# Kernel optimization log

Hardware: AMD Instinct MI355X
Metric: run time of the kernel (lower is better)

## Reference

```python
import jax, jax.numpy as jnp
import numpy as np

B, T, F = 1024, 512, 32
H, E, L = 128, 16, 2
N_TICKERS = 5000


def _gru_layer(x_seq, W_ih, W_hh, b_ih, b_hh):
    # x_seq: [B, T, I]; W_ih: [3H, I]; W_hh: [3H, H]. PyTorch gate order: r, z, n.
    gx = jnp.einsum('bti,gi->btg', x_seq, W_ih) + b_ih  # [B, T, 3H]

    def step(h, gx_t):
        gh = h @ W_hh.T + b_hh                     # [B, 3H]
        r = jax.nn.sigmoid(gx_t[:, :H] + gh[:, :H])
        z = jax.nn.sigmoid(gx_t[:, H:2 * H] + gh[:, H:2 * H])
        n = jnp.tanh(gx_t[:, 2 * H:] + r * gh[:, 2 * H:])
        h_new = (1.0 - z) * n + z * h
        return h_new, h_new

    h0 = jnp.zeros((x_seq.shape[0], H), dtype=x_seq.dtype)
    _, hs = jax.lax.scan(step, h0, jnp.swapaxes(gx, 0, 1))  # hs: [T, B, H]
    return jnp.swapaxes(hs, 0, 1)                            # [B, T, H]


def setup_inputs() -> dict:
    key = jax.random.key(0)
    ks = jax.random.split(key, 16)
    s_in0 = 1.0 / np.sqrt(H)
    inp = {
        'x': jax.random.normal(ks[0], (B, T, F), dtype=jnp.float32),
        'ticker_ids': jax.random.randint(ks[1], (B,), 0, N_TICKERS),
        'embed': jax.random.normal(ks[2], (N_TICKERS, E), dtype=jnp.float32),
        # GRU layer 0 (input size F+E=48)
        'W_ih0': jax.random.uniform(ks[3], (3 * H, F + E), minval=-s_in0, maxval=s_in0),
        'W_hh0': jax.random.uniform(ks[4], (3 * H, H), minval=-s_in0, maxval=s_in0),
        'b_ih0': jax.random.uniform(ks[5], (3 * H,), minval=-s_in0, maxval=s_in0),
        'b_hh0': jax.random.uniform(ks[6], (3 * H,), minval=-s_in0, maxval=s_in0),
        # GRU layer 1 (input size H)
        'W_ih1': jax.random.uniform(ks[7], (3 * H, H), minval=-s_in0, maxval=s_in0),
        'W_hh1': jax.random.uniform(ks[8], (3 * H, H), minval=-s_in0, maxval=s_in0),
        'b_ih1': jax.random.uniform(ks[9], (3 * H,), minval=-s_in0, maxval=s_in0),
        'b_hh1': jax.random.uniform(ks[10], (3 * H,), minval=-s_in0, maxval=s_in0),
        # head: Linear(H,H) -> ReLU -> Linear(H,1)
        'head_w1': jax.random.uniform(ks[11], (H, H), minval=-s_in0, maxval=s_in0),
        'head_b1': jax.random.uniform(ks[12], (H,), minval=-s_in0, maxval=s_in0),
        'head_w2': jax.random.uniform(ks[13], (1, H), minval=-s_in0, maxval=s_in0),
        'head_b2': jax.random.uniform(ks[14], (1,), minval=-s_in0, maxval=s_in0),
    }
    return inp


def reference(x, ticker_ids, embed, W_ih0, W_hh0, b_ih0, b_hh0,
              W_ih1, W_hh1, b_ih1, b_hh1, head_w1, head_b1, head_w2, head_b2):
    emb = embed[ticker_ids]                                  # [B, E]
    emb_seq = jnp.broadcast_to(emb[:, None, :], (x.shape[0], x.shape[1], emb.shape[-1]))
    xcat = jnp.concatenate([x, emb_seq], axis=-1)            # [B, T, F+E]
    h = _gru_layer(xcat, W_ih0, W_hh0, b_ih0, b_hh0)         # [B, T, H]
    h = _gru_layer(h, W_ih1, W_hh1, b_ih1, b_hh1)            # [B, T, H]
    last = h[:, -1, :]                                       # [B, H]
    hid = jax.nn.relu(last @ head_w1.T + head_b1)            # dropout inactive at eval
    y = (hid @ head_w2.T + head_b2)[:, 0]                    # [B]
    return y
```

## Files before the change

kernel.cpp:

```cpp
#include <hip/hip_runtime.h>

constexpr int kB  = 1024;
constexpr int kT  = 512;
constexpr int kF  = 32;
constexpr int kE  = 16;
constexpr int kH  = 128;
constexpr int kMB = 16;
constexpr int kNMB = kB / kMB;
constexpr int kTc = 16;
constexpr int kNCh = kT / kTc;
constexpr int kTg = kTc / 2;
constexpr size_t kH0Str = (size_t)kB * kTc * kH;
constexpr size_t kSlots = (size_t)kNMB * kTc * 512;
constexpr size_t kGx0Str = kSlots * 12;

typedef __attribute__((ext_vector_type(8))) _Float16 f16x8;
typedef __attribute__((ext_vector_type(4))) _Float16 f16x4;
typedef __attribute__((ext_vector_type(4))) float    f32x4;

#define MFMA16(a,b,c) __builtin_amdgcn_mfma_f32_16x16x32_f16(a,b,c,0,0,0)

__device__ __forceinline__ float sigm_hw(float x){
    float e = __builtin_amdgcn_exp2f(-1.442695041f * x);
    return __builtin_amdgcn_rcpf(1.0f + e);
}
__device__ __forceinline__ float tanh_hw(float x){
    float e = __builtin_amdgcn_exp2f(-2.885390082f * x);
    return fmaf(2.0f, __builtin_amdgcn_rcpf(1.0f + e), -1.0f);
}
__device__ __forceinline__ void splitF(float v, _Float16 &hi, _Float16 &lo){
    hi = (_Float16)v;
    lo = (_Float16)(v - (float)hi);
}
__device__ __forceinline__ f16x8 loadW8(const float* __restrict__ p){
    f16x8 r;
#pragma unroll
    for (int j=0;j<8;j++) r[j] = (_Float16)p[j];
    return r;
}
__device__ __forceinline__ unsigned short f2u(_Float16 h){ return __builtin_bit_cast(unsigned short, h); }
__device__ __forceinline__ _Float16 u2f(unsigned short u){ return __builtin_bit_cast(_Float16, u); }
__device__ __forceinline__ unsigned pack2(float a, float b){
    return (unsigned)f2u((_Float16)a) | ((unsigned)f2u((_Float16)b) << 16);
}
__device__ __forceinline__ float uf(unsigned u){ return __builtin_bit_cast(float, u); }
__device__ __forceinline__ void bar_lds(){
    asm volatile("s_waitcnt lgkmcnt(0)\n\ts_barrier" ::: "memory");
}

struct SRec {
    alignas(16) _Float16 hH[2][16][136];
    alignas(16) _Float16 hL[2][16][136];
    alignas(16) float hf[16][132];
    alignas(16) float hf2[16][132];
};
struct SGem {
    alignas(16) _Float16 aH[2][16][136];
    alignas(16) _Float16 aL[2][16][136];
};
union SU { SRec r; SGem g; };

struct G3 { uint4 r, z, n; };

__attribute__((amdgpu_waves_per_eu(2, 2)))
__global__ void __launch_bounds__(512) rnn_fused(
    const float* __restrict__ x, const int* __restrict__ tick,
    const float* __restrict__ embed,
    const float* __restrict__ Wih0, const float* __restrict__ Whh0,
    const float* __restrict__ bih0, const float* __restrict__ bhh0,
    const float* __restrict__ Wih1, const float* __restrict__ bih1,
    const float* __restrict__ Whh1, const float* __restrict__ bhh1,
    const float* __restrict__ hw1, const float* __restrict__ hb1,
    const float* __restrict__ hw2, const float* __restrict__ hb2,
    unsigned* __restrict__ h0seq, unsigned* __restrict__ gxA,
    unsigned* __restrict__ gxB, float* __restrict__ h1state,
    unsigned* __restrict__ gx0, float* __restrict__ out, int c)
{
    __shared__ SU sm;
    const int tid = threadIdx.x;
    const int w = tid >> 6, l = tid & 63, lm = l & 15, lq = l >> 4;
    const int i = 16*w + lm;
    const int cls[3] = { i, 128 + i, 256 + i };

    if (blockIdx.x < 64) {
        if (c < 0 || c >= kNCh) return;
        SRec &S = sm.r;
        const int mb = blockIdx.x;
        unsigned* h0w = h0seq + (size_t)(c & 1) * kH0Str;
        const unsigned* g0 = gx0 + (size_t)(c & 1) * kGx0Str;

        f16x8 wv[3][4];
#pragma unroll
        for (int T=0; T<3; T++)
#pragma unroll
            for (int kt=0; kt<4; kt++)
                wv[T][kt] = loadW8(Whh0 + (size_t)cls[T]*kH + kt*32 + lq*8);
        const float bn = bhh0[cls[2]];

        float hreg[4];
        if (c == 0){
#pragma unroll
            for (int q=0;q<4;q++){
                hreg[q]=0.f;
                S.hH[0][lq*4+q][i]=(_Float16)0.f;
                S.hL[0][lq*4+q][i]=(_Float16)0.f;
            }
        } else {
            const unsigned* h0p = h0seq + (size_t)((c-1) & 1) * kH0Str;
#pragma unroll
            for (int q=0;q<4;q++){
                unsigned u = h0p[((size_t)(mb*kTc + kTc-1)*16 + lq*4+q)*kH + i];
                _Float16 hh = u2f((unsigned short)(u>>16)), hl = u2f((unsigned short)u);
                hreg[q] = (float)hh + (float)hl;
                S.hH[0][lq*4+q][i]=hh; S.hL[0][lq*4+q][i]=hl;
            }
        }
        const size_t base = (size_t)mb*kTc*512 + tid;
        auto ld3 = [&](size_t slot){
            G3 g; const unsigned* p = g0 + slot*12;
            g.r = *(const uint4*)p; g.z = *(const uint4*)(p+4); g.n = *(const uint4*)(p+8);
            return g;
        };
        G3 gc = ld3(base), gn = ld3(base + 512);
        bar_lds();

        int buf = 0;
        for (int tc=0; tc<kTc; tc++){
            const int nb = buf ^ 1;
            f16x8 aHf[4], aLf[4];
#pragma unroll
            for (int kt=0;kt<4;kt++){
                aHf[kt] = *(const f16x8*)&S.hH[buf][lm][kt*32 + lq*8];
                aLf[kt] = *(const f16x8*)&S.hL[buf][lm][kt*32 + lq*8];
            }
            f32x4 aR  = __builtin_bit_cast(f32x4, gc.r);
            f32x4 aZ  = __builtin_bit_cast(f32x4, gc.z);
            f32x4 aNH = {bn,bn,bn,bn};
            f32x4 aRl = {0.f,0.f,0.f,0.f};
            f32x4 aZl = {0.f,0.f,0.f,0.f};
            f32x4 aNl = {0.f,0.f,0.f,0.f};
#pragma unroll
            for (int kt=0;kt<4;kt++){
                aR =MFMA16(aHf[kt],wv[0][kt],aR);  aRl=MFMA16(aLf[kt],wv[0][kt],aRl);
                aZ =MFMA16(aHf[kt],wv[1][kt],aZ);  aZl=MFMA16(aLf[kt],wv[1][kt],aZl);
                aNH=MFMA16(aHf[kt],wv[2][kt],aNH); aNl=MFMA16(aLf[kt],wv[2][kt],aNl);
            }
            aR += aRl; aZ += aZl; aNH += aNl;
            const float nx[4] = { uf(gc.n.x), uf(gc.n.y), uf(gc.n.z), uf(gc.n.w) };
            unsigned pk[4];
#pragma unroll
            for (int q=0;q<4;q++){
                float r = sigm_hw(aR[q]);
                float z = sigm_hw(aZ[q]);
                float n = tanh_hw(fmaf(r, aNH[q], nx[q]));
                float h = fmaf(z, hreg[q]-n, n);
                hreg[q] = h;
                _Float16 hh,hl; splitF(h,hh,hl);
                S.hH[nb][lq*4+q][i]=hh;
                S.hL[nb][lq*4+q][i]=hl;
                pk[q] = ((unsigned)f2u(hh)<<16) | f2u(hl);
            }
#pragma unroll
            for (int q=0;q<4;q++)
                h0w[((size_t)(mb*kTc + tc)*16 + lq*4+q)*kH + i] = pk[q];
            gc = gn;
            int tn = tc + 2; if (tn > kTc-1) tn = kTc-1;
            gn = ld3(base + (size_t)tn*512);
            bar_lds();
            buf = nb;
        }
    } else if (blockIdx.x < 192) {
        const int bid = blockIdx.x - 64;
        const int mb = bid >> 1, t0 = (bid & 1) * kTg;
        const int b0 = mb * kMB;
        const int g = c - 1;
        if (g >= 0 && g < kNCh) {
            SGem &S = sm.g;
            const unsigned* h0r = h0seq + (size_t)(g & 1) * kH0Str;
            unsigned* gA = gxA + (size_t)(g & 1) * kSlots * 4;
            unsigned* gB = gxB + (size_t)(g & 1) * kSlots * 2;

            f16x8 wv[3][4]; float bI[3];
#pragma unroll
            for (int T=0; T<3; T++){
#pragma unroll
                for (int kt=0; kt<4; kt++)
                    wv[T][kt] = loadW8(Wih1 + (size_t)cls[T]*kH + kt*32 + lq*8);
                bI[T] = bih1[cls[T]];
            }
            const int sr = tid >> 5, sq = tid & 31;
            auto ld = [&](int t){
                return *(const uint4*)(h0r + ((size_t)(mb*kTc + t)*16 + sr)*kH + 4*sq);
            };
            auto stage = [&](int bf, uint4 u){
                f16x4 vh = { u2f((unsigned short)(u.x>>16)), u2f((unsigned short)(u.y>>16)),
                             u2f((unsigned short)(u.z>>16)), u2f((unsigned short)(u.w>>16)) };
                f16x4 vl = { u2f((unsigned short)u.x), u2f((unsigned short)u.y),
                             u2f((unsigned short)u.z), u2f((unsigned short)u.w) };
                *(f16x4*)&S.aH[bf][sr][4*sq] = vh;
                *(f16x4*)&S.aL[bf][sr][4*sq] = vl;
            };
            stage(0, ld(t0));
            uint4 nxt = ld(t0 + 1);
            bar_lds();
            for (int tt=0; tt<kTg; tt++){
                const int t = t0 + tt, bf = tt & 1;
                f16x8 fH[4], fL[4];
#pragma unroll
                for (int kt=0;kt<4;kt++){
                    fH[kt] = *(const f16x8*)&S.aH[bf][lm][kt*32 + lq*8];
                    fL[kt] = *(const f16x8*)&S.aL[bf][lm][kt*32 + lq*8];
                }
                if (tt+1 < kTg) stage(bf^1, nxt);
                if (tt+2 < kTg) nxt = ld(t0 + tt + 2);
                f32x4 aR = {bI[0],bI[0],bI[0],bI[0]};
                f32x4 aZ = {bI[1],bI[1],bI[1],bI[1]};
                f32x4 aN = {bI[2],bI[2],bI[2],bI[2]};
#pragma unroll
                for (int kt=0;kt<4;kt++){
                    aR=MFMA16(fH[kt],wv[0][kt],aR); aR=MFMA16(fL[kt],wv[0][kt],aR);
                    aZ=MFMA16(fH[kt],wv[1][kt],aZ); aZ=MFMA16(fL[kt],wv[1][kt],aZ);
                    aN=MFMA16(fH[kt],wv[2][kt],aN); aN=MFMA16(fL[kt],wv[2][kt],aN);
                }
                const size_t slot = ((size_t)mb*kTc + t)*512 + tid;
                *(uint4*)(gA + slot*4) = make_uint4(pack2(aR[0],aR[1]), pack2(aR[2],aR[3]),
                                                    pack2(aZ[0],aZ[1]), pack2(aZ[2],aZ[3]));
                *(uint2*)(gB + slot*2) = make_uint2(pack2(aN[0],aN[1]), pack2(aN[2],aN[3]));
                bar_lds();
            }
        }
        const int p = c + 1;
        if (p >= 0 && p < kNCh) {
            unsigned* g0w = gx0 + (size_t)(p & 1) * kGx0Str;
            f16x8 xw[3];
#pragma unroll
            for (int T=0; T<3; T++)
                xw[T] = loadW8(Wih0 + (size_t)cls[T]*48 + lq*8);
            float ini[3][4];
            {
                const float bi0 = bih0[cls[0]] + bhh0[cls[0]];
                const float bi1 = bih0[cls[1]] + bhh0[cls[1]];
                const float bi2 = bih0[cls[2]];
                const float* w0 = Wih0 + (size_t)cls[0]*48 + 32;
                const float* w1 = Wih0 + (size_t)cls[1]*48 + 32;
                const float* w2 = Wih0 + (size_t)cls[2]*48 + 32;
#pragma unroll
                for (int q=0; q<4; q++){
                    const float* ep = embed + (size_t)tick[b0 + lq*4 + q] * kE;
                    float s0=0.f, s1=0.f, s2=0.f;
#pragma unroll
                    for (int e=0; e<kE; e++){
                        float ev = ep[e];
                        s0 = fmaf(ev, w0[e], s0);
                        s1 = fmaf(ev, w1[e], s1);
                        s2 = fmaf(ev, w2[e], s2);
                    }
                    ini[0][q]=bi0+s0; ini[1][q]=bi1+s1; ini[2][q]=bi2+s2;
                }
            }
            for (int tt=0; tt<kTg; tt++){
                const int t = t0 + tt;
                const float* xp = x + (size_t)(b0+lm)*kT*kF + (size_t)(p*kTc + t)*kF + lq*8;
                const float4 xa = *(const float4*)xp;
                const float4 xb = *(const float4*)(xp + 4);
                const float xv[8] = { xa.x, xa.y, xa.z, xa.w, xb.x, xb.y, xb.z, xb.w };
                f16x8 xH, xL;
#pragma unroll
                for (int j=0;j<8;j++){
                    _Float16 hh,hl; splitF(xv[j],hh,hl);
                    xH[j]=hh; xL[j]=hl;
                }
                f32x4 aR = {ini[0][0],ini[0][1],ini[0][2],ini[0][3]};
                f32x4 aZ = {ini[1][0],ini[1][1],ini[1][2],ini[1][3]};
                f32x4 aN = {ini[2][0],ini[2][1],ini[2][2],ini[2][3]};
                aR=MFMA16(xH,xw[0],aR); aR=MFMA16(xL,xw[0],aR);
                aZ=MFMA16(xH,xw[1],aZ); aZ=MFMA16(xL,xw[1],aZ);
                aN=MFMA16(xH,xw[2],aN); aN=MFMA16(xL,xw[2],aN);
                const size_t slot = ((size_t)mb*kTc + t)*512 + tid;
                *(uint4*)(g0w + slot*12)     = __builtin_bit_cast(uint4, aR);
                *(uint4*)(g0w + slot*12 + 4) = __builtin_bit_cast(uint4, aZ);
                *(uint4*)(g0w + slot*12 + 8) = __builtin_bit_cast(uint4, aN);
            }
        }
    } else {
        const int e0 = c - 2;
        if (e0 < 0 || e0 >= kNCh) return;
        SRec &S = sm.r;
        const int mb = blockIdx.x - 192, b0 = mb * kMB;
        const unsigned* gA = gxA + (size_t)(e0 & 1) * kSlots * 4;
        const unsigned* gB = gxB + (size_t)(e0 & 1) * kSlots * 2;

        f16x8 wv[3][4];
#pragma unroll
        for (int T=0; T<3; T++)
#pragma unroll
            for (int kt=0; kt<4; kt++)
                wv[T][kt] = loadW8(Whh1 + (size_t)cls[T]*kH + kt*32 + lq*8);
        const float br = bhh1[cls[0]], bz = bhh1[cls[1]], bn = bhh1[cls[2]];

        float hreg[4];
        if (e0 == 0){
#pragma unroll
            for (int q=0;q<4;q++){
                hreg[q]=0.f;
                S.hH[0][lq*4+q][i]=(_Float16)0.f;
                S.hL[0][lq*4+q][i]=(_Float16)0.f;
            }
        } else {
#pragma unroll
            for (int q=0;q<4;q++){
                float h = h1state[(size_t)(b0 + lq*4+q)*kH + i];
                hreg[q]=h;
                _Float16 hh,hl; splitF(h,hh,hl);
                S.hH[0][lq*4+q][i]=hh; S.hL[0][lq*4+q][i]=hl;
            }
        }
        const size_t base = (size_t)mb*kTc*512 + tid;
        uint4 g4c = *(const uint4*)(gA + base*4);
        uint2 g2c = *(const uint2*)(gB + base*2);
        uint4 g4n = *(const uint4*)(gA + (base + 512)*4);
        uint2 g2n = *(const uint2*)(gB + (base + 512)*2);
        bar_lds();

        int buf = 0;
        for (int tc=0; tc<kTc; tc++){
            const int nb = buf ^ 1;
            f16x8 aHf[4], aLf[4];
#pragma unroll
            for (int kt=0;kt<4;kt++){
                aHf[kt] = *(const f16x8*)&S.hH[buf][lm][kt*32 + lq*8];
                aLf[kt] = *(const f16x8*)&S.hL[buf][lm][kt*32 + lq*8];
            }
            f32x4 aR={br,br,br,br}, aZ={bz,bz,bz,bz}, aNH={bn,bn,bn,bn};
            f32x4 aRl={0.f,0.f,0.f,0.f}, aZl={0.f,0.f,0.f,0.f}, aNl={0.f,0.f,0.f,0.f};
#pragma unroll
            for (int kt=0;kt<4;kt++){
                aR =MFMA16(aHf[kt],wv[0][kt],aR);  aRl=MFMA16(aLf[kt],wv[0][kt],aRl);
                aZ =MFMA16(aHf[kt],wv[1][kt],aZ);  aZl=MFMA16(aLf[kt],wv[1][kt],aZl);
                aNH=MFMA16(aHf[kt],wv[2][kt],aNH); aNl=MFMA16(aLf[kt],wv[2][kt],aNl);
            }
            aR += aRl; aZ += aZl; aNH += aNl;
            const float rx[4] = { (float)u2f((unsigned short)g4c.x), (float)u2f((unsigned short)(g4c.x>>16)),
                                  (float)u2f((unsigned short)g4c.y), (float)u2f((unsigned short)(g4c.y>>16)) };
            const float zx[4] = { (float)u2f((unsigned short)g4c.z), (float)u2f((unsigned short)(g4c.z>>16)),
                                  (float)u2f((unsigned short)g4c.w), (float)u2f((unsigned short)(g4c.w>>16)) };
            const float nx[4] = { (float)u2f((unsigned short)g2c.x), (float)u2f((unsigned short)(g2c.x>>16)),
                                  (float)u2f((unsigned short)g2c.y), (float)u2f((unsigned short)(g2c.y>>16)) };
#pragma unroll
            for (int q=0;q<4;q++){
                float r = sigm_hw(aR[q] + rx[q]);
                float z = sigm_hw(aZ[q] + zx[q]);
                float n = tanh_hw(fmaf(r, aNH[q], nx[q]));
                float h = fmaf(z, hreg[q]-n, n);
                hreg[q] = h;
                _Float16 hh,hl; splitF(h,hh,hl);
                S.hH[nb][lq*4+q][i]=hh;
                S.hL[nb][lq*4+q][i]=hl;
            }
            g4c = g4n; g2c = g2n;
            int tn = tc + 2; if (tn > kTc-1) tn = kTc-1;
            g4n = *(const uint4*)(gA + (base + (size_t)tn*512)*4);
            g2n = *(const uint2*)(gB + (base + (size_t)tn*512)*2);
            bar_lds();
            buf = nb;
        }
#pragma unroll
        for (int q=0;q<4;q++)
            h1state[(size_t)(b0 + lq*4+q)*kH + i] = hreg[q];
        if (e0 == kNCh-1){
#pragma unroll
            for (int q=0;q<4;q++) S.hf[lq*4+q][i] = hreg[q];
            __syncthreads();
            const int hm = tid >> 5, i0 = (tid & 31) * 4;
#pragma unroll
            for (int e=0;e<4;e++){
                const float* wr = hw1 + (size_t)(i0+e)*kH;
                float s = hb1[i0+e];
                for (int k2=0;k2<kH;k2++) s = fmaf(wr[k2], S.hf[hm][k2], s);
                S.hf2[hm][i0+e] = fmaxf(s, 0.f);
            }
            __syncthreads();
            if (tid < kMB){
                float s = hb2[0];
                for (int k2=0;k2<kH;k2++) s = fmaf(S.hf2[tid][k2], hw2[k2], s);
                out[b0 + tid] = s;
            }
        }
    }
}

extern "C" void kernel_launch(void* const* d_in, const int* in_sizes, int n_in,
                              void* d_out, int out_size, void* d_ws, size_t ws_size,
                              hipStream_t stream)
{
    const float* x     = (const float*)d_in[0];
    const int*   tick  = (const int*)d_in[1];
    const float* embed = (const float*)d_in[2];
    const float* Wih0  = (const float*)d_in[3];
    const float* Whh0  = (const float*)d_in[4];
    const float* bih0  = (const float*)d_in[5];
    const float* bhh0  = (const float*)d_in[6];
    const float* Wih1  = (const float*)d_in[7];
    const float* Whh1  = (const float*)d_in[8];
    const float* bih1  = (const float*)d_in[9];
    const float* bhh1  = (const float*)d_in[10];
    const float* hw1   = (const float*)d_in[11];
    const float* hb1   = (const float*)d_in[12];
    const float* hw2   = (const float*)d_in[13];
    const float* hb2   = (const float*)d_in[14];
    float* out = (float*)d_out;

    unsigned* h0seq = (unsigned*)d_ws;
    unsigned* gxA   = h0seq + 2*kH0Str;
    unsigned* gxB   = gxA + 2*kSlots*4;
    float*  h1state = (float*)(gxB + 2*kSlots*2);
    unsigned* gx0   = (unsigned*)(h1state + (size_t)kB*kH);

    for (int c = -1; c <= kNCh + 1; c++){
        rnn_fused<<<256, 512, 0, stream>>>(x, tick, embed,
            Wih0, Whh0, bih0, bhh0, Wih1, bih1, Whh1, bhh1,
            hw1, hb1, hw2, hb2, h0seq, gxA, gxB, h1state, gx0, out, c);
    }
}
```

Measured before the change: 1.274 ms.

## Convert per-chunk kernel launches into one persistent cooperative kernel with grid sync

Replaces the host loop of one launch per time chunk with a single cooperative launch. Each block keeps its weights and hidden state in registers and LDS across chunks and uses grid.sync between pipeline stages. This removes repeated launch overhead, repeated weight and constant reloads, and the global round trip of the carried hidden state. The chunk length is also doubled, so there are half as many stages and syncs, at the cost of larger workspace buffers and a longer pipeline fill and drain. Grid-wide barriers need every block co-resident and add their own per-stage latency.

```diff
diff --git a/kernel.cpp b/kernel.cpp
--- a/kernel.cpp
+++ b/kernel.cpp
@@ -1,4 +1,6 @@
 #include <hip/hip_runtime.h>
+#include <hip/hip_cooperative_groups.h>
+namespace cg = cooperative_groups;
 
 constexpr int kB  = 1024;
 constexpr int kT  = 512;
@@ -7,7 +9,7 @@
 constexpr int kH  = 128;
 constexpr int kMB = 16;
 constexpr int kNMB = kB / kMB;
-constexpr int kTc = 16;
+constexpr int kTc = 32;
 constexpr int kNCh = kT / kTc;
 constexpr int kTg = kTc / 2;
 constexpr size_t kH0Str = (size_t)kB * kTc * kH;
@@ -63,7 +65,7 @@
 struct G3 { uint4 r, z, n; };
 
 __attribute__((amdgpu_waves_per_eu(2, 2)))
-__global__ void __launch_bounds__(512) rnn_fused(
+__global__ void __launch_bounds__(512) rnn_persist(
     const float* __restrict__ x, const int* __restrict__ tick,
     const float* __restrict__ embed,
     const float* __restrict__ Wih0, const float* __restrict__ Whh0,
@@ -73,22 +75,19 @@
     const float* __restrict__ hw1, const float* __restrict__ hb1,
     const float* __restrict__ hw2, const float* __restrict__ hb2,
     unsigned* __restrict__ h0seq, unsigned* __restrict__ gxA,
-    unsigned* __restrict__ gxB, float* __restrict__ h1state,
-    unsigned* __restrict__ gx0, float* __restrict__ out, int c)
+    unsigned* __restrict__ gxB, unsigned* __restrict__ gx0,
+    float* __restrict__ out)
 {
     __shared__ SU sm;
+    cg::grid_group grid = cg::this_grid();
     const int tid = threadIdx.x;
     const int w = tid >> 6, l = tid & 63, lm = l & 15, lq = l >> 4;
     const int i = 16*w + lm;
     const int cls[3] = { i, 128 + i, 256 + i };
 
     if (blockIdx.x < 64) {
-        if (c < 0 || c >= kNCh) return;
         SRec &S = sm.r;
         const int mb = blockIdx.x;
-        unsigned* h0w = h0seq + (size_t)(c & 1) * kH0Str;
-        const unsigned* g0 = gx0 + (size_t)(c & 1) * kGx0Str;
-
         f16x8 wv[3][4];
 #pragma unroll
         for (int T=0; T<3; T++)
@@ -98,198 +97,191 @@
         const float bn = bhh0[cls[2]];
 
         float hreg[4];
-        if (c == 0){
-#pragma unroll
-            for (int q=0;q<4;q++){
-                hreg[q]=0.f;
-                S.hH[0][lq*4+q][i]=(_Float16)0.f;
-                S.hL[0][lq*4+q][i]=(_Float16)0.f;
+#pragma unroll
+        for (int q=0;q<4;q++){
+            hreg[q]=0.f;
+            S.hH[0][lq*4+q][i]=(_Float16)0.f;
+            S.hL[0][lq*4+q][i]=(_Float16)0.f;
+        }
+        const size_t base = (size_t)mb*kTc*512 + tid;
+        int buf = 0;
+        for (int c = -1; c <= kNCh+1; ++c){
+            if (c >= 0 && c < kNCh){
+                unsigned* h0w = h0seq + (size_t)(c & 1) * kH0Str;
+                const unsigned* g0 = gx0 + (size_t)(c & 1) * kGx0Str;
+                auto ld3 = [&](size_t slot){
+                    G3 g; const unsigned* p = g0 + slot*12;
+                    g.r = *(const uint4*)p; g.z = *(const uint4*)(p+4); g.n = *(const uint4*)(p+8);
+                    return g;
+                };
+                G3 gc = ld3(base), gn = ld3(base + 512);
+                bar_lds();
+                for (int tc=0; tc<kTc; tc++){
+                    const int nb = buf ^ 1;
+                    f16x8 aHf[4], aLf[4];
+#pragma unroll
+                    for (int kt=0;kt<4;kt++){
+                        aHf[kt] = *(const f16x8*)&S.hH[buf][lm][kt*32 + lq*8];
+                        aLf[kt] = *(const f16x8*)&S.hL[buf][lm][kt*32 + lq*8];
+                    }
+                    f32x4 aR  = __builtin_bit_cast(f32x4, gc.r);
+                    f32x4 aZ  = __builtin_bit_cast(f32x4, gc.z);
+                    f32x4 aNH = {bn,bn,bn,bn};
+                    f32x4 aRl = {0.f,0.f,0.f,0.f};
+                    f32x4 aZl = {0.f,0.f,0.f,0.f};
+                    f32x4 aNl = {0.f,0.f,0.f,0.f};
+#pragma unroll
+                    for (int kt=0;kt<4;kt++){
+                        aR =MFMA16(aHf[kt],wv[0][kt],aR);  aRl=MFMA16(aLf[kt],wv[0][kt],aRl);
+                        aZ =MFMA16(aHf[kt],wv[1][kt],aZ);  aZl=MFMA16(aLf[kt],wv[1][kt],aZl);
+                        aNH=MFMA16(aHf[kt],wv[2][kt],aNH); aNl=MFMA16(aLf[kt],wv[2][kt],aNl);
+                    }
+                    aR += aRl; aZ += aZl; aNH += aNl;
+                    const float nx[4] = { uf(gc.n.x), uf(gc.n.y), uf(gc.n.z), uf(gc.n.w) };
+                    unsigned pk[4];
+#pragma unroll
+                    for (int q=0;q<4;q++){
+                        float r = sigm_hw(aR[q]);
+                        float z = sigm_hw(aZ[q]);
+                        float n = tanh_hw(fmaf(r, aNH[q], nx[q]));
+                        float h = fmaf(z, hreg[q]-n, n);
+                        hreg[q] = h;
+                        _Float16 hh,hl; splitF(h,hh,hl);
+                        S.hH[nb][lq*4+q][i]=hh;
+                        S.hL[nb][lq*4+q][i]=hl;
+                        pk[q] = ((unsigned)f2u(hh)<<16) | f2u(hl);
+                    }
+#pragma unroll
+                    for (int q=0;q<4;q++)
+                        h0w[((size_t)(mb*kTc + tc)*16 + lq*4+q)*kH + i] = pk[q];
+                    gc = gn;
+                    int tn = tc + 2; if (tn > kTc-1) tn = kTc-1;
+                    gn = ld3(base + (size_t)tn*512);
+                    bar_lds();
+                    buf = nb;
+                }
             }
-        } else {
-            const unsigned* h0p = h0seq + (size_t)((c-1) & 1) * kH0Str;
-#pragma unroll
-            for (int q=0;q<4;q++){
-                unsigned u = h0p[((size_t)(mb*kTc + kTc-1)*16 + lq*4+q)*kH + i];
-                _Float16 hh = u2f((unsigned short)(u>>16)), hl = u2f((unsigned short)u);
-                hreg[q] = (float)hh + (float)hl;
-                S.hH[0][lq*4+q][i]=hh; S.hL[0][lq*4+q][i]=hl;
-            }
-        }
-        const size_t base = (size_t)mb*kTc*512 + tid;
-        auto ld3 = [&](size_t slot){
-            G3 g; const unsigned* p = g0 + slot*12;
-            g.r = *(const uint4*)p; g.z = *(const uint4*)(p+4); g.n = *(const uint4*)(p+8);
-            return g;
-        };
-        G3 gc = ld3(base), gn = ld3(base + 512);
-        bar_lds();
-
-        int buf = 0;
-        for (int tc=0; tc<kTc; tc++){
-            const int nb = buf ^ 1;
-            f16x8 aHf[4], aLf[4];
-#pragma unroll
-            for (int kt=0;kt<4;kt++){
-                aHf[kt] = *(const f16x8*)&S.hH[buf][lm][kt*32 + lq*8];
-                aLf[kt] = *(const f16x8*)&S.hL[buf][lm][kt*32 + lq*8];
-            }
-            f32x4 aR  = __builtin_bit_cast(f32x4, gc.r);
-            f32x4 aZ  = __builtin_bit_cast(f32x4, gc.z);
-            f32x4 aNH = {bn,bn,bn,bn};
-            f32x4 aRl = {0.f,0.f,0.f,0.f};
-            f32x4 aZl = {0.f,0.f,0.f,0.f};
-            f32x4 aNl = {0.f,0.f,0.f,0.f};
-#pragma unroll
-            for (int kt=0;kt<4;kt++){
-                aR =MFMA16(aHf[kt],wv[0][kt],aR);  aRl=MFMA16(aLf[kt],wv[0][kt],aRl);
-                aZ =MFMA16(aHf[kt],wv[1][kt],aZ);  aZl=MFMA16(aLf[kt],wv[1][kt],aZl);
-                aNH=MFMA16(aHf[kt],wv[2][kt],aNH); aNl=MFMA16(aLf[kt],wv[2][kt],aNl);
-            }
-            aR += aRl; aZ += aZl; aNH += aNl;
-            const float nx[4] = { uf(gc.n.x), uf(gc.n.y), uf(gc.n.z), uf(gc.n.w) };
-            unsigned pk[4];
-#pragma unroll
-            for (int q=0;q<4;q++){
-                float r = sigm_hw(aR[q]);
-                float z = sigm_hw(aZ[q]);
-                float n = tanh_hw(fmaf(r, aNH[q], nx[q]));
-                float h = fmaf(z, hreg[q]-n, n);
-                hreg[q] = h;
-                _Float16 hh,hl; splitF(h,hh,hl);
-                S.hH[nb][lq*4+q][i]=hh;
-                S.hL[nb][lq*4+q][i]=hl;
-                pk[q] = ((unsigned)f2u(hh)<<16) | f2u(hl);
-            }
-#pragma unroll
-            for (int q=0;q<4;q++)
-                h0w[((size_t)(mb*kTc + tc)*16 + lq*4+q)*kH + i] = pk[q];
-            gc = gn;
-            int tn = tc + 2; if (tn > kTc-1) tn = kTc-1;
-            gn = ld3(base + (size_t)tn*512);
-            bar_lds();
-            buf = nb;
+            if (c <= kNCh){ __threadfence(); grid.sync(); __threadfence(); }
         }
     } else if (blockIdx.x < 192) {
         const int bid = blockIdx.x - 64;
         const int mb = bid >> 1, t0 = (bid & 1) * kTg;
         const int b0 = mb * kMB;
-        const int g = c - 1;
-        if (g >= 0 && g < kNCh) {
-            SGem &S = sm.g;
-            const unsigned* h0r = h0seq + (size_t)(g & 1) * kH0Str;
-            unsigned* gA = gxA + (size_t)(g & 1) * kSlots * 4;
-            unsigned* gB = gxB + (size_t)(g & 1) * kSlots * 2;
-
-            f16x8 wv[3][4]; float bI[3];
-#pragma unroll
-            for (int T=0; T<3; T++){
-#pragma unroll
-                for (int kt=0; kt<4; kt++)
-                    wv[T][kt] = loadW8(Wih1 + (size_t)cls[T]*kH + kt*32 + lq*8);
-                bI[T] = bih1[cls[T]];
+        SGem &S = sm.g;
+        f16x8 wv1[3][4]; float bI[3];
+#pragma unroll
+        for (int T=0; T<3; T++){
+#pragma unroll
+            for (int kt=0; kt<4; kt++)
+                wv1[T][kt] = loadW8(Wih1 + (size_t)cls[T]*kH + kt*32 + lq*8);
+            bI[T] = bih1[cls[T]];
+        }
+        f16x8 xw[3];
+#pragma unroll
+        for (int T=0; T<3; T++)
+            xw[T] = loadW8(Wih0 + (size_t)cls[T]*48 + lq*8);
+        float ini[3][4];
+        {
+            const float bi0 = bih0[cls[0]] + bhh0[cls[0]];
+            const float bi1 = bih0[cls[1]] + bhh0[cls[1]];
+            const float bi2 = bih0[cls[2]];
+            const float* w0 = Wih0 + (size_t)cls[0]*48 + 32;
+            const float* w1 = Wih0 + (size_t)cls[1]*48 + 32;
+            const float* w2 = Wih0 + (size_t)cls[2]*48 + 32;
+#pragma unroll
+            for (int q=0; q<4; q++){
+                const float* ep = embed + (size_t)tick[b0 + lq*4 + q] * kE;
+                float s0=0.f, s1=0.f, s2=0.f;
+#pragma unroll
+                for (int e=0; e<kE; e++){
+                    float ev = ep[e];
+                    s0 = fmaf(ev, w0[e], s0);
+                    s1 = fmaf(ev, w1[e], s1);
+                    s2 = fmaf(ev, w2[e], s2);
+                }
+                ini[0][q]=bi0+s0; ini[1][q]=bi1+s1; ini[2][q]=bi2+s2;
             }
-            const int sr = tid >> 5, sq = tid & 31;
-            auto ld = [&](int t){
-                return *(const uint4*)(h0r + ((size_t)(mb*kTc + t)*16 + sr)*kH + 4*sq);
-            };
-            auto stage = [&](int bf, uint4 u){
-                f16x4 vh = { u2f((unsigned short)(u.x>>16)), u2f((unsigned short)(u.y>>16)),
-                             u2f((unsigned short)(u.z>>16)), u2f((unsigned short)(u.w>>16)) };
-                f16x4 vl = { u2f((unsigned short)u.x), u2f((unsigned short)u.y),
-                             u2f((unsigned short)u.z), u2f((unsigned short)u.w) };
-                *(f16x4*)&S.aH[bf][sr][4*sq] = vh;
-                *(f16x4*)&S.aL[bf][sr][4*sq] = vl;
-            };
-            stage(0, ld(t0));
-            uint4 nxt = ld(t0 + 1);
-            bar_lds();
-            for (int tt=0; tt<kTg; tt++){
-                const int t = t0 + tt, bf = tt & 1;
-                f16x8 fH[4], fL[4];
-#pragma unroll
-                for (int kt=0;kt<4;kt++){
-                    fH[kt] = *(const f16x8*)&S.aH[bf][lm][kt*32 + lq*8];
-                    fL[kt] = *(const f16x8*)&S.aL[bf][lm][kt*32 + lq*8];
-                }
-                if (tt+1 < kTg) stage(bf^1, nxt);
-                if (tt+2 < kTg) nxt = ld(t0 + tt + 2);
-                f32x4 aR = {bI[0],bI[0],bI[0],bI[0]};
-                f32x4 aZ = {bI[1],bI[1],bI[1],bI[1]};
-                f32x4 aN = {bI[2],bI[2],bI[2],bI[2]};
-#pragma unroll
-                for (int kt=0;kt<4;kt++){
-                    aR=MFMA16(fH[kt],wv[0][kt],aR); aR=MFMA16(fL[kt],wv[0][kt],aR);
-                    aZ=MFMA16(fH[kt],wv[1][kt],aZ); aZ=MFMA16(fL[kt],wv[1][kt],aZ);
-                    aN=MFMA16(fH[kt],wv[2][kt],aN); aN=MFMA16(fL[kt],wv[2][kt],aN);
-                }
-                const size_t slot = ((size_t)mb*kTc + t)*512 + tid;
-                *(uint4*)(gA + slot*4) = make_uint4(pack2(aR[0],aR[1]), pack2(aR[2],aR[3]),
-                                                    pack2(aZ[0],aZ[1]), pack2(aZ[2],aZ[3]));
-                *(uint2*)(gB + slot*2) = make_uint2(pack2(aN[0],aN[1]), pack2(aN[2],aN[3]));
+        }
+        const int sr = tid >> 5, sq = tid & 31;
+
+        for (int c = -1; c <= kNCh+1; ++c){
+            const int g = c - 1;
+            if (g >= 0 && g < kNCh) {
+                const unsigned* h0r = h0seq + (size_t)(g & 1) * kH0Str;
+                unsigned* gA = gxA + (size_t)(g & 1) * kSlots * 4;
+                unsigned* gB = gxB + (size_t)(g & 1) * kSlots * 2;
+                auto ld = [&](int t){
+                    return *(const uint4*)(h0r + ((size_t)(mb*kTc + t)*16 + sr)*kH + 4*sq);
+                };
+                auto stage = [&](int bf, uint4 u){
+                    f16x4 vh = { u2f((unsigned short)(u.x>>16)), u2f((unsigned short)(u.y>>16)),
+                                 u2f((unsigned short)(u.z>>16)), u2f((unsigned short)(u.w>>16)) };
+                    f16x4 vl = { u2f((unsigned short)u.x), u2f((unsigned short)u.y),
+                                 u2f((unsigned short)u.z), u2f((unsigned short)u.w) };
+                    *(f16x4*)&S.aH[bf][sr][4*sq] = vh;
+                    *(f16x4*)&S.aL[bf][sr][4*sq] = vl;
+                };
+                stage(0, ld(t0));
+                uint4 nxt = ld(t0 + 1);
                 bar_lds();
+                for (int tt=0; tt<kTg; tt++){
+                    const int t = t0 + tt, bf = tt & 1;
+                    f16x8 fH[4], fL[4];
+#pragma unroll
+                    for (int kt=0;kt<4;kt++){
+                        fH[kt] = *(const f16x8*)&S.aH[bf][lm][kt*32 + lq*8];
+                        fL[kt] = *(const f16x8*)&S.aL[bf][lm][kt*32 + lq*8];
+                    }
+                    if (tt+1 < kTg) stage(bf^1, nxt);
+                    if (tt+2 < kTg) nxt = ld(t0 + tt + 2);
+                    f32x4 aR = {bI[0],bI[0],bI[0],bI[0]};
+                    f32x4 aZ = {bI[1],bI[1],bI[1],bI[1]};
+                    f32x4 aN = {bI[2],bI[2],bI[2],bI[2]};
+#pragma unroll
+                    for (int kt=0;kt<4;kt++){
+                        aR=MFMA16(fH[kt],wv1[0][kt],aR); aR=MFMA16(fL[kt],wv1[0][kt],aR);
+                        aZ=MFMA16(fH[kt],wv1[1][kt],aZ); aZ=MFMA16(fL[kt],wv1[1][kt],aZ);
+                        aN=MFMA16(fH[kt],wv1[2][kt],aN); aN=MFMA16(fL[kt],wv1[2][kt],aN);
+                    }
+                    const size_t slot = ((size_t)mb*kTc + t)*512 + tid;
+                    *(uint4*)(gA + slot*4) = make_uint4(pack2(aR[0],aR[1]), pack2(aR[2],aR[3]),
+                                                        pack2(aZ[0],aZ[1]), pack2(aZ[2],aZ[3]));
+                    *(uint2*)(gB + slot*2) = make_uint2(pack2(aN[0],aN[1]), pack2(aN[2],aN[3]));
+                    bar_lds();
+                }
             }
-        }
-        const int p = c + 1;
-        if (p >= 0 && p < kNCh) {
-            unsigned* g0w = gx0 + (size_t)(p & 1) * kGx0Str;
-            f16x8 xw[3];
-#pragma unroll
-            for (int T=0; T<3; T++)
-                xw[T] = loadW8(Wih0 + (size_t)cls[T]*48 + lq*8);
-            float ini[3][4];
-            {
-                const float bi0 = bih0[cls[0]] + bhh0[cls[0]];
-                const float bi1 = bih0[cls[1]] + bhh0[cls[1]];
-                const float bi2 = bih0[cls[2]];
-                const float* w0 = Wih0 + (size_t)cls[0]*48 + 32;
-                const float* w1 = Wih0 + (size_t)cls[1]*48 + 32;
-                const float* w2 = Wih0 + (size_t)cls[2]*48 + 32;
-#pragma unroll
-                for (int q=0; q<4; q++){
-                    const float* ep = embed + (size_t)tick[b0 + lq*4 + q] * kE;
-                    float s0=0.f, s1=0.f, s2=0.f;
-#pragma unroll
-                    for (int e=0; e<kE; e++){
-                        float ev = ep[e];
-                        s0 = fmaf(ev, w0[e], s0);
-                        s1 = fmaf(ev, w1[e], s1);
-                        s2 = fmaf(ev, w2[e], s2);
-                    }
-                    ini[0][q]=bi0+s0; ini[1][q]=bi1+s1; ini[2][q]=bi2+s2;
+            const int p = c + 1;
+            if (p >= 0 && p < kNCh) {
+                unsigned* g0w = gx0 + (size_t)(p & 1) * kGx0Str;
+                for (int tt=0; tt<kTg; tt++){
+                    const int t = t0 + tt;
+                    const float* xp = x + (size_t)(b0+lm)*kT*kF + (size_t)(p*kTc + t)*kF + lq*8;
+                    const float4 xa = *(const float4*)xp;
+                    const float4 xb = *(const float4*)(xp + 4);
+                    const float xv[8] = { xa.x, xa.y, xa.z, xa.w, xb.x, xb.y, xb.z, xb.w };
+                    f16x8 xH, xL;
+#pragma unroll
+                    for (int j=0;j<8;j++){
+                        _Float16 hh,hl; splitF(xv[j],hh,hl);
+                        xH[j]=hh; xL[j]=hl;
+                    }
+                    f32x4 aR = {ini[0][0],ini[0][1],ini[0][2],ini[0][3]};
+                    f32x4 aZ = {ini[1][0],ini[1][1],ini[1][2],ini[1][3]};
+                    f32x4 aN = {ini[2][0],ini[2][1],ini[2][2],ini[2][3]};
+                    aR=MFMA16(xH,xw[0],aR); aR=MFMA16(xL,xw[0],aR);
+                    aZ=MFMA16(xH,xw[1],aZ); aZ=MFMA16(xL,xw[1],aZ);
+                    aN=MFMA16(xH,xw[2],aN); aN=MFMA16(xL,xw[2],aN);
+                    const size_t slot = ((size_t)mb*kTc + t)*512 + tid;
+                    *(uint4*)(g0w + slot*12)     = __builtin_bit_cast(uint4, aR);
+                    *(uint4*)(g0w + slot*12 + 4) = __builtin_bit_cast(uint4, aZ);
+                    *(uint4*)(g0w + slot*12 + 8) = __builtin_bit_cast(uint4, aN);
                 }
             }
-            for (int tt=0; tt<kTg; tt++){
-                const int t = t0 + tt;
-                const float* xp = x + (size_t)(b0+lm)*kT*kF + (size_t)(p*kTc + t)*kF + lq*8;
-                const float4 xa = *(const float4*)xp;
-                const float4 xb = *(const float4*)(xp + 4);
-                const float xv[8] = { xa.x, xa.y, xa.z, xa.w, xb.x, xb.y, xb.z, xb.w };
-                f16x8 xH, xL;
-#pragma unroll
-                for (int j=0;j<8;j++){
-                    _Float16 hh,hl; splitF(xv[j],hh,hl);
-                    xH[j]=hh; xL[j]=hl;
-                }
-                f32x4 aR = {ini[0][0],ini[0][1],ini[0][2],ini[0][3]};
-                f32x4 aZ = {ini[1][0],ini[1][1],ini[1][2],ini[1][3]};
-                f32x4 aN = {ini[2][0],ini[2][1],ini[2][2],ini[2][3]};
-                aR=MFMA16(xH,xw[0],aR); aR=MFMA16(xL,xw[0],aR);
-                aZ=MFMA16(xH,xw[1],aZ); aZ=MFMA16(xL,xw[1],aZ);
-                aN=MFMA16(xH,xw[2],aN); aN=MFMA16(xL,xw[2],aN);
-                const size_t slot = ((size_t)mb*kTc + t)*512 + tid;
-                *(uint4*)(g0w + slot*12)     = __builtin_bit_cast(uint4, aR);
-                *(uint4*)(g0w + slot*12 + 4) = __builtin_bit_cast(uint4, aZ);
-                *(uint4*)(g0w + slot*12 + 8) = __builtin_bit_cast(uint4, aN);
-            }
+            if (c <= kNCh){ __threadfence(); grid.sync(); __threadfence(); }
         }
     } else {
-        const int e0 = c - 2;
-        if (e0 < 0 || e0 >= kNCh) return;
         SRec &S = sm.r;
         const int mb = blockIdx.x - 192, b0 = mb * kMB;
-        const unsigned* gA = gxA + (size_t)(e0 & 1) * kSlots * 4;
-        const unsigned* gB = gxB + (size_t)(e0 & 1) * kSlots * 2;
-
         f16x8 wv[3][4];
 #pragma unroll
         for (int T=0; T<3; T++)
@@ -299,92 +291,89 @@
         const float br = bhh1[cls[0]], bz = bhh1[cls[1]], bn = bhh1[cls[2]];
 
         float hreg[4];
-        if (e0 == 0){
-#pragma unroll
-            for (int q=0;q<4;q++){
-                hreg[q]=0.f;
-                S.hH[0][lq*4+q][i]=(_Float16)0.f;
-                S.hL[0][lq*4+q][i]=(_Float16)0.f;
+        const size_t base = (size_t)mb*kTc*512 + tid;
+        int buf = 0;
+        for (int c = -1; c <= kNCh+1; ++c){
+            const int e0 = c - 2;
+            if (e0 >= 0 && e0 < kNCh){
+                if (e0 == 0){
+                    buf = 0;
+#pragma unroll
+                    for (int q=0;q<4;q++){
+                        hreg[q]=0.f;
+                        S.hH[0][lq*4+q][i]=(_Float16)0.f;
+                        S.hL[0][lq*4+q][i]=(_Float16)0.f;
+                    }
+                }
+                const unsigned* gA = gxA + (size_t)(e0 & 1) * kSlots * 4;
+                const unsigned* gB = gxB + (size_t)(e0 & 1) * kSlots * 2;
+                uint4 g4c = *(const uint4*)(gA + base*4);
+                uint2 g2c = *(const uint2*)(gB + base*2);
+                uint4 g4n = *(const uint4*)(gA + (base + 512)*4);
+                uint2 g2n = *(const uint2*)(gB + (base + 512)*2);
+                bar_lds();
+                for (int tc=0; tc<kTc; tc++){
+                    const int nb = buf ^ 1;
+                    f16x8 aHf[4], aLf[4];
+#pragma unroll
+                    for (int kt=0;kt<4;kt++){
+                        aHf[kt] = *(const f16x8*)&S.hH[buf][lm][kt*32 + lq*8];
+                        aLf[kt] = *(const f16x8*)&S.hL[buf][lm][kt*32 + lq*8];
+                    }
+                    f32x4 aR={br,br,br,br}, aZ={bz,bz,bz,bz}, aNH={bn,bn,bn,bn};
+                    f32x4 aRl={0.f,0.f,0.f,0.f}, aZl={0.f,0.f,0.f,0.f}, aNl={0.f,0.f,0.f,0.f};
+#pragma unroll
+                    for (int kt=0;kt<4;kt++){
+                        aR =MFMA16(aHf[kt],wv[0][kt],aR);  aRl=MFMA16(aLf[kt],wv[0][kt],aRl);
+                        aZ =MFMA16(aHf[kt],wv[1][kt],aZ);  aZl=MFMA16(aLf[kt],wv[1][kt],aZl);
+                        aNH=MFMA16(aHf[kt],wv[2][kt],aNH); aNl=MFMA16(aLf[kt],wv[2][kt],aNl);
+                    }
+                    aR += aRl; aZ += aZl; aNH += aNl;
+                    const float rx[4] = { (float)u2f((unsigned short)g4c.x), (float)u2f((unsigned short)(g4c.x>>16)),
+                                          (float)u2f((unsigned short)g4c.y), (float)u2f((unsigned short)(g4c.y>>16)) };
+                    const float zx[4] = { (float)u2f((unsigned short)g4c.z), (float)u2f((unsigned short)(g4c.z>>16)),
+                                          (float)u2f((unsigned short)g4c.w), (float)u2f((unsigned short)(g4c.w>>16)) };
+                    const float nx[4] = { (float)u2f((unsigned short)g2c.x), (float)u2f((unsigned short)(g2c.x>>16)),
+                                          (float)u2f((unsigned short)g2c.y), (float)u2f((unsigned short)(g2c.y>>16)) };
+#pragma unroll
+                    for (int q=0;q<4;q++){
+                        float r = sigm_hw(aR[q] + rx[q]);
+                        float z = sigm_hw(aZ[q] + zx[q]);
+                        float n = tanh_hw(fmaf(r, aNH[q], nx[q]));
+                        float h = fmaf(z, hreg[q]-n, n);
+                        hreg[q] = h;
+                        _Float16 hh,hl; splitF(h,hh,hl);
+                        S.hH[nb][lq*4+q][i]=hh;
+                        S.hL[nb][lq*4+q][i]=hl;
+                    }
+                    g4c = g4n; g2c = g2n;
+                    int tn = tc + 2; if (tn > kTc-1) tn = kTc-1;
+                    g4n = *(const uint4*)(gA + (base + (size_t)tn*512)*4);
+                    g2n = *(const uint2*)(gB + (base + (size_t)tn*512)*2);
+                    bar_lds();
+                    buf = nb;
+                }
+                if (e0 == kNCh-1){
+#pragma unroll
+                    for (int q=0;q<4;q++) S.hf[lq*4+q][i] = hreg[q];
+                    __syncthreads();
+                    const int hm = tid >> 5, i0 = (tid & 31) * 4;
+#pragma unroll
+                    for (int e=0;e<4;e++){
+                        const float* wr = hw1 + (size_t)(i0+e)*kH;
+                        float s = hb1[i0+e];
+                        for (int k2=0;k2<kH;k2++) s = fmaf(wr[k2], S.hf[hm][k2], s);
+                        S.hf2[hm][i0+e] = fmaxf(s, 0.f);
+                    }
+                    __syncthreads();
+                    if (tid < kMB){
+                        float s = hb2[0];
+                        for (int k2=0;k2<kH;k2++) s = fmaf(S.hf2[tid][k2], hw2[k2], s);
+                        out[b0 + tid] = s;
+                    }
+                }
             }
-        } else {
-#pragma unroll
-            for (int q=0;q<4;q++){
-                float h = h1state[(size_t)(b0 + lq*4+q)*kH + i];
-                hreg[q]=h;
-                _Float16 hh,hl; splitF(h,hh,hl);
-                S.hH[0][lq*4+q][i]=hh; S.hL[0][lq*4+q][i]=hl;
-            }
-        }
-        const size_t base = (size_t)mb*kTc*512 + tid;
-        uint4 g4c = *(const uint4*)(gA + base*4);
-        uint2 g2c = *(const uint2*)(gB + base*2);
-        uint4 g4n = *(const uint4*)(gA + (base + 512)*4);
-        uint2 g2n = *(const uint2*)(gB + (base + 512)*2);
-        bar_lds();
-
-        int buf = 0;
-        for (int tc=0; tc<kTc; tc++){
-            const int nb = buf ^ 1;
-            f16x8 aHf[4], aLf[4];
-#pragma unroll
-            for (int kt=0;kt<4;kt++){
-                aHf[kt] = *(const f16x8*)&S.hH[buf][lm][kt*32 + lq*8];
-                aLf[kt] = *(const f16x8*)&S.hL[buf][lm][kt*32 + lq*8];
-            }
-            f32x4 aR={br,br,br,br}, aZ={bz,bz,bz,bz}, aNH={bn,bn,bn,bn};
-            f32x4 aRl={0.f,0.f,0.f,0.f}, aZl={0.f,0.f,0.f,0.f}, aNl={0.f,0.f,0.f,0.f};
-#pragma unroll
-            for (int kt=0;kt<4;kt++){
-                aR =MFMA16(aHf[kt],wv[0][kt],aR);  aRl=MFMA16(aLf[kt],wv[0][kt],aRl);
-                aZ =MFMA16(aHf[kt],wv[1][kt],aZ);  aZl=MFMA16(aLf[kt],wv[1][kt],aZl);
-                aNH=MFMA16(aHf[kt],wv[2][kt],aNH); aNl=MFMA16(aLf[kt],wv[2][kt],aNl);
-            }
-            aR += aRl; aZ += aZl; aNH += aNl;
-            const float rx[4] = { (float)u2f((unsigned short)g4c.x), (float)u2f((unsigned short)(g4c.x>>16)),
-                                  (float)u2f((unsigned short)g4c.y), (float)u2f((unsigned short)(g4c.y>>16)) };
-            const float zx[4] = { (float)u2f((unsigned short)g4c.z), (float)u2f((unsigned short)(g4c.z>>16)),
-                                  (float)u2f((unsigned short)g4c.w), (float)u2f((unsigned short)(g4c.w>>16)) };
-            const float nx[4] = { (float)u2f((unsigned short)g2c.x), (float)u2f((unsigned short)(g2c.x>>16)),
-                                  (float)u2f((unsigned short)g2c.y), (float)u2f((unsigned short)(g2c.y>>16)) };
-#pragma unroll
-            for (int q=0;q<4;q++){
-                float r = sigm_hw(aR[q] + rx[q]);
-                float z = sigm_hw(aZ[q] + zx[q]);
-                float n = tanh_hw(fmaf(r, aNH[q], nx[q]));
-                float h = fmaf(z, hreg[q]-n, n);
-                hreg[q] = h;
-                _Float16 hh,hl; splitF(h,hh,hl);
-                S.hH[nb][lq*4+q][i]=hh;
-                S.hL[nb][lq*4+q][i]=hl;
-            }
-            g4c = g4n; g2c = g2n;
-            int tn = tc + 2; if (tn > kTc-1) tn = kTc-1;
-            g4n = *(const uint4*)(gA + (base + (size_t)tn*512)*4);
-            g2n = *(const uint2*)(gB + (base + (size_t)tn*512)*2);
-            bar_lds();
-            buf = nb;
-        }
-#pragma unroll
-        for (int q=0;q<4;q++)
-            h1state[(size_t)(b0 + lq*4+q)*kH + i] = hreg[q];
-        if (e0 == kNCh-1){
-#pragma unroll
-            for (int q=0;q<4;q++) S.hf[lq*4+q][i] = hreg[q];
-            __syncthreads();
-            const int hm = tid >> 5, i0 = (tid & 31) * 4;
-#pragma unroll
-            for (int e=0;e<4;e++){
-                const float* wr = hw1 + (size_t)(i0+e)*kH;
-                float s = hb1[i0+e];
-                for (int k2=0;k2<kH;k2++) s = fmaf(wr[k2], S.hf[hm][k2], s);
-                S.hf2[hm][i0+e] = fmaxf(s, 0.f);
-            }
-            __syncthreads();
-            if (tid < kMB){
-                float s = hb2[0];
-                for (int k2=0;k2<kH;k2++) s = fmaf(S.hf2[tid][k2], hw2[k2], s);
-                out[b0 + tid] = s;
-            }
+            if (c <= kNCh){ __threadfence(); grid.sync(); __threadfence(); }
         }
     }
 }
@@ -413,12 +402,15 @@
     unsigned* h0seq = (unsigned*)d_ws;
     unsigned* gxA   = h0seq + 2*kH0Str;
     unsigned* gxB   = gxA + 2*kSlots*4;
-    float*  h1state = (float*)(gxB + 2*kSlots*2);
-    unsigned* gx0   = (unsigned*)(h1state + (size_t)kB*kH);
-
-    for (int c = -1; c <= kNCh + 1; c++){
-        rnn_fused<<<256, 512, 0, stream>>>(x, tick, embed,
-            Wih0, Whh0, bih0, bhh0, Wih1, bih1, Whh1, bhh1,
-            hw1, hb1, hw2, hb2, h0seq, gxA, gxB, h1state, gx0, out, c);
-    }
-}
+    unsigned* gx0   = gxB + 2*kSlots*2;
+
+    void* args[] = {
+        (void*)&x, (void*)&tick, (void*)&embed,
+        (void*)&Wih0, (void*)&Whh0, (void*)&bih0, (void*)&bhh0,
+        (void*)&Wih1, (void*)&bih1, (void*)&Whh1, (void*)&bhh1,
+        (void*)&hw1, (void*)&hb1, (void*)&hw2, (void*)&hb2,
+        (void*)&h0seq, (void*)&gxA, (void*)&gxB, (void*)&gx0, (void*)&out
+    };
+    hipLaunchCooperativeKernel((void*)rnn_persist, dim3(256), dim3(512),
+                               args, 0, stream);
+}
```

Measured after the change: 3.299 ms. +159.0%, slower.
